# Kernel tuning notes

Hardware: AMD Instinct MI355X
Metric: run time of the kernel (lower is better)

The kernel has to match this reference:

```python
import jax, jax.numpy as jnp
import numpy as np

N_NODES = 100000
N_EDGES = 640000
D_IN = 128
D_OUT = 128


def setup_inputs() -> dict:
    key = jax.random.key(0)
    k1, k2, k3, k4, k5, k6 = jax.random.split(key, 6)
    x = jax.random.normal(k1, (N_NODES, D_IN), dtype=jnp.float32)
    edge_weights = jax.random.uniform(k2, (N_EDGES, 1), dtype=jnp.float32)
    src = jax.random.randint(k3, (N_EDGES,), 0, N_NODES)
    dst = jax.random.randint(k4, (N_EDGES,), 0, N_NODES)
    # nn.Linear init scale ~ 1/sqrt(in_feats)
    W = jax.random.normal(k5, (D_OUT, D_IN), dtype=jnp.float32) / np.sqrt(D_IN)
    b = jax.random.normal(k6, (D_OUT,), dtype=jnp.float32) / np.sqrt(D_IN)
    return {"x": x, "edge_weights": edge_weights, "src": src, "dst": dst, "W": W, "b": b}


def reference(x, edge_weights, src, dst, W, b):
    # message: gather source node features, scale by per-edge weight  [E, D]
    m = x[src] * edge_weights
    # reduce: sum messages into destination nodes  [N, D]
    h = jax.ops.segment_sum(m, dst, num_segments=N_NODES)
    # dense linear  [N, D_OUT]
    return h @ W.T + b
```

## Files before the change

### kernel.cpp

```cpp
#include <hip/hip_runtime.h>
#include <hip/hip_bf16.h>

#define D 128
#define SCAN_CH 4096

typedef __bf16 bf16x8 __attribute__((ext_vector_type(8)));
typedef float  f32x4  __attribute__((ext_vector_type(4)));
typedef float  f32x2  __attribute__((ext_vector_type(2)));

__device__ __forceinline__ __bf16 f2bf(float f) { return (__bf16)f; }
__device__ __forceinline__ int pad8(int v) { return (v + 7) & ~7; }

__global__ __launch_bounds__(256) void prep_kernel(
    const float* __restrict__ W, __bf16* __restrict__ wb,
    int* __restrict__ cnt, int M, int4* __restrict__ bins4, long nbin4)
{
    long t    = (long)blockIdx.x * 256 + threadIdx.x;
    long nthr = (long)gridDim.x * 256;

    for (long i = t; i < nbin4; i += nthr) bins4[i] = make_int4(0, 0, 0, 0);
    for (long i = t; i < M; i += nthr) cnt[i] = 0;

    if (t < 2048) {
        int lane = (int)t & 63;
        int frag = (int)t >> 6;
        int kb = frag >> 3, fn = frag & 7;
        int n  = fn * 16 + (lane & 15);
        int k0 = kb * 32 + (lane >> 4) * 8;
        const float* src = &W[(size_t)n * D + k0];
        float4 v0 = *reinterpret_cast<const float4*>(src);
        float4 v1 = *reinterpret_cast<const float4*>(src + 4);
        bf16x8 o;
        o[0]=f2bf(v0.x); o[1]=f2bf(v0.y); o[2]=f2bf(v0.z); o[3]=f2bf(v0.w);
        o[4]=f2bf(v1.x); o[5]=f2bf(v1.y); o[6]=f2bf(v1.z); o[7]=f2bf(v1.w);
        *reinterpret_cast<bf16x8*>(&wb[((size_t)frag * 64 + lane) * 8]) = o;
    }
}

__global__ __launch_bounds__(256) void convhist_kernel(
    const float* __restrict__ x, __bf16* __restrict__ xb, long n8,
    const int* __restrict__ dst, int* __restrict__ cnt,
    int* __restrict__ rank, int E, int convBlocks)
{
    const int tid = threadIdx.x;

    if ((int)blockIdx.x < convBlocks) {
        long i = (long)blockIdx.x * 256 + tid;
        if (i < n8) {
            const f32x4* ap = reinterpret_cast<const f32x4*>(&x[i * 8]);
            f32x4 v0 = ap[0];
            f32x4 v1 = ap[1];
            bf16x8 o;
            o[0]=f2bf(v0[0]); o[1]=f2bf(v0[1]); o[2]=f2bf(v0[2]); o[3]=f2bf(v0[3]);
            o[4]=f2bf(v1[0]); o[5]=f2bf(v1[1]); o[6]=f2bf(v1[2]); o[7]=f2bf(v1[3]);
            *reinterpret_cast<bf16x8*>(&xb[i * 8]) = o;
        }
        return;
    }

    int e = ((int)blockIdx.x - convBlocks) * 256 + tid;
    if (e < E) {
        int d = __builtin_nontemporal_load(&dst[e]);
        rank[e] = atomicAdd(&cnt[d], 1);
    }
}

__global__ __launch_bounds__(256) void scan_part_kernel(
    const int* __restrict__ cnt, int* __restrict__ bsum, int N)
{
    __shared__ int wred[4];
    const int tid  = threadIdx.x;
    const int lane = tid & 63;
    const int wid  = tid >> 6;
    int off = blockIdx.x * SCAN_CH + tid * 16;
    int s = 0;
    #pragma unroll
    for (int i = 0; i < 16; ++i) {
        int idx = off + i;
        if (idx < N) s += pad8(cnt[idx]);
    }
    #pragma unroll
    for (int d = 32; d >= 1; d >>= 1) s += __shfl_xor(s, d, 64);
    if (lane == 0) wred[wid] = s;
    __syncthreads();
    if (tid == 0) bsum[blockIdx.x] = wred[0] + wred[1] + wred[2] + wred[3];
}

__global__ __launch_bounds__(256) void scan_write_kernel(
    const int* __restrict__ cnt, const int* __restrict__ bsum,
    int* __restrict__ base, int N, int NB)
{
    __shared__ int boff_s;
    __shared__ int wsum[4];
    const int b    = blockIdx.x;
    const int tid  = threadIdx.x;
    const int lane = tid & 63;
    const int wid  = tid >> 6;

    if (wid == 0) {
        int v = (lane < b) ? bsum[lane] : 0;
        #pragma unroll
        for (int d = 32; d >= 1; d >>= 1) v += __shfl_xor(v, d, 64);
        if (lane == 0) boff_s = v;
    }
    __syncthreads();

    int off = b * SCAN_CH + tid * 16;
    int v[16];
    int s = 0;
    #pragma unroll
    for (int i = 0; i < 16; ++i) {
        int idx = off + i;
        v[i] = (idx < N) ? pad8(cnt[idx]) : 0;
        s += v[i];
    }
    int ssum = s;
    #pragma unroll
    for (int d = 1; d < 64; d <<= 1) {
        int t = __shfl_up(ssum, d, 64);
        if (lane >= d) ssum += t;
    }
    if (lane == 63) wsum[wid] = ssum;
    __syncthreads();
    int woff = 0;
    for (int w = 0; w < wid; ++w) woff += wsum[w];

    int run = boff_s + woff + ssum - s;
    #pragma unroll
    for (int i = 0; i < 16; ++i) {
        int idx = off + i;
        if (idx < N) base[idx] = run;
        if (idx == N - 1) base[N] = run + v[i];
        run += v[i];
    }
}

__global__ __launch_bounds__(256) void bingemm_kernel(
    const __bf16* __restrict__ xb, const __bf16* __restrict__ wb,
    __bf16* __restrict__ y, int M, int gemmBlocks,
    const int* __restrict__ src, const int* __restrict__ dst,
    const float* __restrict__ ew, const int* __restrict__ base,
    const int* __restrict__ rank, int2* __restrict__ bins, int E)
{
    const int tid = threadIdx.x;

    if ((int)blockIdx.x >= gemmBlocks) {
        int e = ((int)blockIdx.x - gemmBlocks) * 256 + tid;
        if (e < E) {
            int d   = __builtin_nontemporal_load(&dst[e]);
            int sv  = __builtin_nontemporal_load(&src[e]);
            float w = __builtin_nontemporal_load(&ew[e]);
            int rk  = __builtin_nontemporal_load(&rank[e]);
            int p = base[d] + rk;
            bins[p] = make_int2(sv * (D / 2), __float_as_int(w));
        }
        return;
    }

    const int lane = tid & 63;
    const int wv   = tid >> 6;
    const int l15  = lane & 15;
    const int l4   = lane >> 4;
    const int row_base = blockIdx.x * 128 + wv * 32;
    if (row_base >= M) return;

    f32x4 acc[2][8];
    #pragma unroll
    for (int mi = 0; mi < 2; ++mi)
        #pragma unroll
        for (int fn = 0; fn < 8; ++fn)
            #pragma unroll
            for (int c = 0; c < 4; ++c) acc[mi][fn][c] = 0.f;

    #pragma unroll
    for (int kb = 0; kb < 4; ++kb) {
        bf16x8 b[8];
        #pragma unroll
        for (int fn = 0; fn < 8; ++fn)
            b[fn] = *reinterpret_cast<const bf16x8*>(
                        &wb[((size_t)(kb * 8 + fn) * 64 + lane) * 8]);
        #pragma unroll
        for (int mi = 0; mi < 2; ++mi) {
            int row = row_base + mi * 16 + l15;
            int rc  = row < M ? row : M - 1;
            bf16x8 a = *reinterpret_cast<const bf16x8*>(
                           &xb[(size_t)rc * D + kb * 32 + l4 * 8]);
            #pragma unroll
            for (int fn = 0; fn < 8; ++fn)
                acc[mi][fn] = __builtin_amdgcn_mfma_f32_16x16x32_bf16(
                                  a, b[fn], acc[mi][fn], 0, 0, 0);
        }
    }

    #pragma unroll
    for (int mi = 0; mi < 2; ++mi)
        #pragma unroll
        for (int r = 0; r < 4; ++r) {
            int row = row_base + mi * 16 + l4 * 4 + r;
            if (row >= M) continue;
            #pragma unroll
            for (int fn = 0; fn < 8; ++fn)
                y[(size_t)row * D + fn * 16 + l15] = f2bf(acc[mi][fn][r]);
        }
}

__global__ __launch_bounds__(256) void gather_kernel(
    const __bf16* __restrict__ y, const int* __restrict__ base,
    const int2* __restrict__ bins, const float* __restrict__ bias,
    float* __restrict__ out, int N)
{
    int gw   = (blockIdx.x * 256 + threadIdx.x) >> 6;
    int lane = threadIdx.x & 63;
    if (gw >= N) return;

    const unsigned* yb = reinterpret_cast<const unsigned*>(y);
    const int b0 = __builtin_amdgcn_readfirstlane(base[gw]);
    const int b1 = __builtin_amdgcn_readfirstlane(base[gw + 1]);
    float accx = 0.f, accy = 0.f;

    for (int i = b0; i < b1; i += 8) {
        int2 e[8];
        #pragma unroll
        for (int t = 0; t < 8; ++t) e[t] = bins[i + t];
        unsigned p[8];
        #pragma unroll
        for (int t = 0; t < 8; ++t)
            p[t] = yb[(unsigned)e[t].x + lane];
        #pragma unroll
        for (int t = 0; t < 8; ++t) {
            float w = __int_as_float(e[t].y);
            accx += __uint_as_float(p[t] << 16) * w;
            accy += __uint_as_float(p[t] & 0xFFFF0000u) * w;
        }
    }

    float2 bv = *reinterpret_cast<const float2*>(&bias[lane * 2]);
    f32x2 o;
    o[0] = accx + bv.x;
    o[1] = accy + bv.y;
    __builtin_nontemporal_store(o, reinterpret_cast<f32x2*>(&out[(size_t)gw * D + lane * 2]));
}

extern "C" void kernel_launch(void* const* d_in, const int* in_sizes, int n_in,
                              void* d_out, int out_size, void* d_ws, size_t ws_size,
                              hipStream_t stream) {
    const float* x   = (const float*)d_in[0];
    const float* ew  = (const float*)d_in[1];
    const int*   src = (const int*)d_in[2];
    const int*   dst = (const int*)d_in[3];
    const float* W   = (const float*)d_in[4];
    const float* b   = (const float*)d_in[5];
    float*       out = (float*)d_out;

    const int E  = in_sizes[2];
    const int M  = out_size / D;
    const int NB = (M + SCAN_CH - 1) / SCAN_CH;
    const size_t BIN_CAP = ((size_t)E + 7 * (size_t)M + 8) & ~(size_t)1;
    const long   N8      = (long)M * D / 8;

    char* p = (char*)d_ws;
    __bf16* y    = (__bf16*)p;             p += (size_t)M * D * 2;
    __bf16* xb   = (__bf16*)p;             p += (size_t)M * D * 2;
    __bf16* wb   = (__bf16*)p;             p += (size_t)32 * 64 * 8 * 2;
    int2*   bins = (int2*)p;               p += BIN_CAP * 8;
    int*    base = (int*)p;                p += (size_t)(M + 1) * 4;
    int*    cnt  = (int*)p;                p += (size_t)M * 4;
    int*    rank = (int*)p;                p += (size_t)E * 4;
    int*    bsum = (int*)p;

    prep_kernel<<<512, 256, 0, stream>>>(W, wb, cnt, M,
                                         (int4*)bins, (long)(BIN_CAP / 2));

    int convBlocks = (int)((N8 + 255) / 256);
    int histBlocks = (E + 255) / 256;
    convhist_kernel<<<convBlocks + histBlocks, 256, 0, stream>>>(
        x, xb, N8, dst, cnt, rank, E, convBlocks);

    scan_part_kernel<<<NB, 256, 0, stream>>>(cnt, bsum, M);
    scan_write_kernel<<<NB, 256, 0, stream>>>(cnt, bsum, base, M, NB);

    int gemmBlocks = (M + 127) / 128;
    int binBlocks  = (E + 255) / 256;
    bingemm_kernel<<<gemmBlocks + binBlocks, 256, 0, stream>>>(
        xb, wb, y, M, gemmBlocks, src, dst, ew, base, rank, bins, E);

    gather_kernel<<<(M * 64 + 255) / 256, 256, 0, stream>>>(y, base, bins, b, out, M);
}
```

Measured before the change: 125.5 us.

## Interleave conversion and histogram blocks, move bin zeroing into convhist

Bin zeroing moves out of the prep kernel into the convhist kernel, so the smaller prep kernel only clears counts and packs W. Convhist now alternates odd blocks (atomic histogram over dst) with even blocks (grid-stride x-to-bf16 conversion plus bin zeroing), so the memory-bound streaming work overlaps the atomic-bound histogram. The conversion now runs on histBlocks blocks, fewer than the old one-block-per-chunk layout. Each of those threads loops over several chunks, which could change load balance.

New measurement: 115.2 us. 8.2% less time.

```diff
diff --git a/kernel.cpp b/kernel.cpp
--- a/kernel.cpp
+++ b/kernel.cpp
@@ -13,17 +13,14 @@
 
 __global__ __launch_bounds__(256) void prep_kernel(
     const float* __restrict__ W, __bf16* __restrict__ wb,
-    int* __restrict__ cnt, int M, int4* __restrict__ bins4, long nbin4)
-{
-    long t    = (long)blockIdx.x * 256 + threadIdx.x;
-    long nthr = (long)gridDim.x * 256;
-
-    for (long i = t; i < nbin4; i += nthr) bins4[i] = make_int4(0, 0, 0, 0);
-    for (long i = t; i < M; i += nthr) cnt[i] = 0;
+    int* __restrict__ cnt, int M)
+{
+    int t = blockIdx.x * 256 + threadIdx.x;
+    for (int i = t; i < M; i += gridDim.x * 256) cnt[i] = 0;
 
     if (t < 2048) {
-        int lane = (int)t & 63;
-        int frag = (int)t >> 6;
+        int lane = t & 63;
+        int frag = t >> 6;
         int kb = frag >> 3, fn = frag & 7;
         int n  = fn * 16 + (lane & 15);
         int k0 = kb * 32 + (lane >> 4) * 8;
@@ -39,30 +36,35 @@
 
 __global__ __launch_bounds__(256) void convhist_kernel(
     const float* __restrict__ x, __bf16* __restrict__ xb, long n8,
+    int4* __restrict__ bins4, long nbin4,
     const int* __restrict__ dst, int* __restrict__ cnt,
-    int* __restrict__ rank, int E, int convBlocks)
-{
-    const int tid = threadIdx.x;
-
-    if ((int)blockIdx.x < convBlocks) {
-        long i = (long)blockIdx.x * 256 + tid;
-        if (i < n8) {
-            const f32x4* ap = reinterpret_cast<const f32x4*>(&x[i * 8]);
-            f32x4 v0 = ap[0];
-            f32x4 v1 = ap[1];
-            bf16x8 o;
-            o[0]=f2bf(v0[0]); o[1]=f2bf(v0[1]); o[2]=f2bf(v0[2]); o[3]=f2bf(v0[3]);
-            o[4]=f2bf(v1[0]); o[5]=f2bf(v1[1]); o[6]=f2bf(v1[2]); o[7]=f2bf(v1[3]);
-            *reinterpret_cast<bf16x8*>(&xb[i * 8]) = o;
+    int* __restrict__ rank, int E, int histBlocks)
+{
+    const int tid  = threadIdx.x;
+    const int half = (int)blockIdx.x >> 1;
+
+    if (blockIdx.x & 1) {
+        int e = half * 256 + tid;
+        if (e < E) {
+            int d = __builtin_nontemporal_load(&dst[e]);
+            rank[e] = atomicAdd(&cnt[d], 1);
         }
         return;
     }
 
-    int e = ((int)blockIdx.x - convBlocks) * 256 + tid;
-    if (e < E) {
-        int d = __builtin_nontemporal_load(&dst[e]);
-        rank[e] = atomicAdd(&cnt[d], 1);
-    }
+    long t    = (long)half * 256 + tid;
+    long nthr = (long)histBlocks * 256;
+    for (long i = t; i < n8; i += nthr) {
+        const f32x4* ap = reinterpret_cast<const f32x4*>(&x[i * 8]);
+        f32x4 v0 = ap[0];
+        f32x4 v1 = ap[1];
+        bf16x8 o;
+        o[0]=f2bf(v0[0]); o[1]=f2bf(v0[1]); o[2]=f2bf(v0[2]); o[3]=f2bf(v0[3]);
+        o[4]=f2bf(v1[0]); o[5]=f2bf(v1[1]); o[6]=f2bf(v1[2]); o[7]=f2bf(v1[3]);
+        *reinterpret_cast<bf16x8*>(&xb[i * 8]) = o;
+    }
+    for (long i = t; i < nbin4; i += nthr)
+        bins4[i] = make_int4(0, 0, 0, 0);
 }
 
 __global__ __launch_bounds__(256) void scan_part_kernel(
@@ -268,13 +270,11 @@
     int*    rank = (int*)p;                p += (size_t)E * 4;
     int*    bsum = (int*)p;
 
-    prep_kernel<<<512, 256, 0, stream>>>(W, wb, cnt, M,
-                                         (int4*)bins, (long)(BIN_CAP / 2));
-
-    int convBlocks = (int)((N8 + 255) / 256);
+    prep_kernel<<<512, 256, 0, stream>>>(W, wb, cnt, M);
+
     int histBlocks = (E + 255) / 256;
-    convhist_kernel<<<convBlocks + histBlocks, 256, 0, stream>>>(
-        x, xb, N8, dst, cnt, rank, E, convBlocks);
+    convhist_kernel<<<2 * histBlocks, 256, 0, stream>>>(
+        x, xb, N8, (int4*)bins, (long)(BIN_CAP / 2), dst, cnt, rank, E, histBlocks);
 
     scan_part_kernel<<<NB, 256, 0, stream>>>(cnt, bsum, M);
     scan_write_kernel<<<NB, 256, 0, stream>>>(cnt, bsum, base, M, NB);
```
